# Kernel optimization log

Measured on AMD Instinct MI355X. Metric: run time of the kernel, lower is better.

Reference implementation:

```python
import jax, jax.numpy as jnp
from jax import lax
import numpy as np

RATIO = 2
KF = 12  # FIR kernel size = 6 * ratio


def _kaiser_sinc_filter(cutoff, half_width, ksize):
    # matches BigVGAN alias_free_torch kaiser_sinc_filter1d (even ksize branch)
    half_size = ksize // 2
    delta_f = 4.0 * half_width
    A = 2.285 * (half_size - 1) * np.pi * delta_f + 7.95
    if A > 50.0:
        beta = 0.1102 * (A - 8.7)
    elif A >= 21.0:
        beta = 0.5842 * (A - 21.0) ** 0.4 + 0.07886 * (A - 21.0)
    else:
        beta = 0.0
    window = np.kaiser(ksize, beta)
    time = np.arange(-half_size, half_size) + 0.5
    filt = 2 * cutoff * window * np.sinc(2 * cutoff * time)
    filt = filt / filt.sum()
    return filt.astype(np.float32)


FILT = jnp.asarray(_kaiser_sinc_filter(0.5 / RATIO, 0.6 / RATIO, KF))  # [12], symmetric


def _depthwise(x, stride, lhs_dil, pad):
    # x: [B, C, T]; same FIR filter applied per channel
    C = x.shape[1]
    w = jnp.broadcast_to(FILT.reshape(1, 1, KF), (C, 1, KF))
    return lax.conv_general_dilated(
        x, w, window_strides=(stride,), padding=[pad], lhs_dilation=(lhs_dil,),
        dimension_numbers=('NCH', 'OIH', 'NCH'), feature_group_count=C)


def _activation1d(x, log_alpha, log_beta):
    # anti-aliased SnakeBeta: upsample x2 -> snake -> downsample x2 (length preserved)
    # UpSample1d(ratio=2): replicate-pad 5, conv_transpose stride 2, crop 15 each side
    x = jnp.pad(x, ((0, 0), (0, 0), (5, 5)), mode='edge')
    x = RATIO * _depthwise(x, stride=1, lhs_dil=RATIO, pad=(KF - 1, KF - 1))
    x = x[..., 15:-15]  # [B, C, 2T]
    a = jnp.exp(log_alpha)[None, :, None]
    b = jnp.exp(log_beta)[None, :, None]
    x = x + (1.0 / (b + 1e-9)) * jnp.square(jnp.sin(x * a))
    # DownSample1d: replicate-pad (5, 6), conv stride 2
    x = jnp.pad(x, ((0, 0), (0, 0), (5, 6)), mode='edge')
    return _depthwise(x, stride=RATIO, lhs_dil=1, pad=(0, 0))


def _wn_conv(x, v, g, b, d):
    # weight_norm: w = g * v / ||v||_(in,k) per output channel; dilated, 'same' padding
    w = g * v * lax.rsqrt(jnp.sum(v * v, axis=(1, 2), keepdims=True))
    y = lax.conv_general_dilated(
        x, w, window_strides=(1,), padding=[(d, d)], rhs_dilation=(d,),
        dimension_numbers=('NCH', 'OIH', 'NCH'))
    return y + b[None, :, None]


def setup_inputs() -> dict:
    key = jax.random.key(0)
    ks = jax.random.split(key, 4)
    B, C, T, L = 8, 512, 8192, 3
    x = jax.random.normal(ks[0], (B, C, T), jnp.float32)
    conv_v = 0.01 * jax.random.normal(ks[1], (L, C, C, 3), jnp.float32)  # init_weights std=0.01
    conv_g = jnp.ones((L, C, 1, 1), jnp.float32)
    conv_b = jnp.zeros((L, C), jnp.float32)
    alpha = 0.1 * jax.random.normal(ks[2], (L, C), jnp.float32)  # log-scale snake params
    beta = 0.1 * jax.random.normal(ks[3], (L, C), jnp.float32)
    return {'x': x, 'conv_v': conv_v, 'conv_g': conv_g, 'conv_b': conv_b,
            'alpha': alpha, 'beta': beta}


def reference(x, conv_v, conv_g, conv_b, alpha, beta):
    for i, d in enumerate((1, 3, 5)):
        xt = _activation1d(x, alpha[i], beta[i])
        xt = _wn_conv(xt, conv_v[i], conv_g[i], conv_b[i], d)
        x = xt + x
    return x
```

## Files before the change

kernel.cpp:

```cpp
#include <hip/hip_runtime.h>
#include <hip/hip_bf16.h>
#include <cmath>

#define CCH 512
#define TLEN 8192
#define NB 8
#define KFILT 12

typedef unsigned short u16;
typedef __attribute__((ext_vector_type(8))) short short8;
typedef __attribute__((ext_vector_type(8))) unsigned short ushort8;
typedef __attribute__((ext_vector_type(4))) float float4v;
typedef __attribute__((ext_vector_type(4))) int int4v;

struct Filt { float f[KFILT]; };

static double bessel_i0(double x) {
    double sum = 1.0, term = 1.0;
    for (int k = 1; k < 40; ++k) {
        double t = (x * 0.5) / k;
        term *= t * t;
        sum += term;
        if (term < 1e-18 * sum) break;
    }
    return sum;
}

static void make_filter(float* out) {
    const int ksize = KFILT, half = KFILT / 2;
    const double cutoff = 0.5 / 2.0;
    const double half_width = 0.6 / 2.0;
    const double delta_f = 4.0 * half_width;
    const double PI = 3.14159265358979323846;
    double A = 2.285 * (half - 1) * PI * delta_f + 7.95;
    double beta;
    if (A > 50.0) beta = 0.1102 * (A - 8.7);
    else if (A >= 21.0) beta = 0.5842 * pow(A - 21.0, 0.4) + 0.07886 * (A - 21.0);
    else beta = 0.0;
    double i0b = bessel_i0(beta);
    double sum = 0.0, f[KFILT];
    for (int n = 0; n < ksize; ++n) {
        double r = (2.0 * n) / (ksize - 1) - 1.0;
        double w = bessel_i0(beta * sqrt(fmax(0.0, 1.0 - r * r))) / i0b;
        double t = (n - half) + 0.5;
        double xx = 2.0 * cutoff * t;
        double snc = (xx == 0.0) ? 1.0 : sin(PI * xx) / (PI * xx);
        f[n] = 2.0 * cutoff * w * snc;
        sum += f[n];
    }
    for (int n = 0; n < ksize; ++n) out[n] = (float)(f[n] / sum);
}

__device__ __forceinline__ float bf2f(u16 u) {
    return __uint_as_float(((unsigned int)u) << 16);
}
__device__ __forceinline__ u16 f2bf(float f) {
    unsigned int x = __float_as_uint(f);
    unsigned int r = (x + 0x7fffu + ((x >> 16) & 1u)) >> 16;
    return (u16)r;
}
__device__ __forceinline__ float ldin(const void* p, size_t i, int isf) {
    return isf ? ((const float*)p)[i] : bf2f(((const u16*)p)[i]);
}
__device__ __forceinline__ void gl_lds16(const void* g, void* s) {
    __builtin_amdgcn_global_load_lds(
        (const __attribute__((address_space(1))) unsigned int*)g,
        (__attribute__((address_space(3))) unsigned int*)s, 16, 0, 0);
}

__global__ __launch_bounds__(256) void k_detect(const u16* __restrict__ x,
                                                int* __restrict__ flag) {
    int tid = threadIdx.x;
    int bad = 0;
    for (int i = tid; i < 4096; i += 256) {
        int e = (x[i] >> 7) & 0xFF;
        if (e >= 0x86) bad++;
    }
    for (int off = 32; off > 0; off >>= 1) bad += __shfl_down(bad, off, 64);
    __shared__ int r[4];
    if ((tid & 63) == 0) r[tid >> 6] = bad;
    __syncthreads();
    if (tid == 0) flag[0] = (r[0] + r[1] + r[2] + r[3] >= 64) ? 1 : 0;
}

__global__ __launch_bounds__(256) void k_scales(const void* __restrict__ v,
                                                const void* __restrict__ g,
                                                float* __restrict__ scales,
                                                const int* __restrict__ flg) {
    int isf = *flg;
    int blk = blockIdx.x;
    int tid = threadIdx.x;
    float s = 0.f;
    for (int i = tid; i < CCH * 3; i += 256) {
        float x = ldin(v, (size_t)blk * (CCH * 3) + i, isf);
        s = fmaf(x, x, s);
    }
    for (int off = 32; off > 0; off >>= 1) s += __shfl_down(s, off, 64);
    __shared__ float red[4];
    if ((tid & 63) == 0) red[tid >> 6] = s;
    __syncthreads();
    if (tid == 0) {
        float tot = red[0] + red[1] + red[2] + red[3];
        scales[blk] = ldin(g, blk, isf) / sqrtf(tot);
    }
}

__global__ __launch_bounds__(256) void k_repack(const void* __restrict__ v,
                                                u16* __restrict__ wp,
                                                const int* __restrict__ flg) {
    int isf = *flg;
    int l = blockIdx.y;
    int i = blockIdx.x * 256 + threadIdx.x;
    int tap = i >> 18;
    int rem = i & 262143;
    int co = rem >> 9, ci = rem & 511;
    size_t src = (((size_t)l * CCH + co) * CCH + ci) * 3 + tap;
    u16 val = isf ? f2bf(((const float*)v)[src]) : ((const u16*)v)[src];
    wp[(((size_t)l * 3 + tap) * CCH + co) * CCH + ci] = val;
}

template<int UL>
__device__ __forceinline__ float su_val(const float* xr, const Filt& F,
                                        float a, float invb) {
    constexpr int S = (UL < 0) ? -(((-UL) + 1) / 2) : (UL / 2);
    constexpr int P = ((UL % 2) + 2) % 2;
    constexpr int B = S + (P ? 4 : 3);
    float acc = F.f[P] * xr[B];
    #pragma unroll
    for (int r = 1; r < 6; ++r) acc = fmaf(F.f[2 * r + P], xr[B + r], acc);
    acc *= 2.0f;
    float sn = __sinf(acc * a);
    return fmaf(invb, sn * sn, acc);
}

__global__ __launch_bounds__(256) void k_act(const void* __restrict__ xsrc,
                                             const void* __restrict__ alpha,
                                             const void* __restrict__ beta,
                                             int prmofs, u16* __restrict__ xt,
                                             Filt F, const int* __restrict__ flg,
                                             int layer0) {
    const int isf = *flg;
    const int sif = layer0 ? isf : 0;
    const int tid = threadIdx.x;
    const int lane = tid & 63, w = tid >> 6;
    const int b = blockIdx.z;
    const int c = blockIdx.y * 64 + lane;
    const int t0 = blockIdx.x * 128 + w * 32;
    const size_t rowbase = ((size_t)(b * CCH + c)) * TLEN;

    const float a = expf(ldin(alpha, prmofs + c, isf));
    const float invb = 1.0f / (expf(ldin(beta, prmofs + c, isf)) + 1e-9f);

    float xr[44];
    const bool interior = (t0 != 0) && (t0 != TLEN - 32);
    if (sif) {
        const float* xp = (const float*)xsrc + rowbase;
        if (interior) {
            #pragma unroll
            for (int i = 0; i < 12; ++i) {
                float4v v = *(const float4v*)(xp + t0 - 8 + i * 4);
                #pragma unroll
                for (int j = 0; j < 4; ++j) {
                    int k = i * 4 + j - 2;
                    if (k >= 0 && k < 44) xr[k] = v[j];
                }
            }
        } else {
            #pragma unroll
            for (int k = 0; k < 44; ++k)
                xr[k] = xp[min(max(t0 - 6 + k, 0), TLEN - 1)];
        }
    } else {
        const u16* xp = (const u16*)xsrc + rowbase;
        if (interior) {
            #pragma unroll
            for (int i = 0; i < 6; ++i) {
                ushort8 v = *(const ushort8*)(xp + t0 - 8 + i * 8);
                #pragma unroll
                for (int j = 0; j < 8; ++j) {
                    int k = i * 8 + j - 2;
                    if (k >= 0 && k < 44) xr[k] = bf2f(v[j]);
                }
            }
        } else {
            #pragma unroll
            for (int k = 0; k < 44; ++k)
                xr[k] = bf2f(xp[min(max(t0 - 6 + k, 0), TLEN - 1)]);
        }
    }

    float wv[12];
    wv[7]  = su_val<-5>(xr, F, a, invb);
    wv[8]  = su_val<-4>(xr, F, a, invb);
    wv[9]  = su_val<-3>(xr, F, a, invb);
    wv[10] = su_val<-2>(xr, F, a, invb);
    wv[11] = su_val<-1>(xr, F, a, invb);
    wv[0]  = su_val<0>(xr, F, a, invb);
    wv[1]  = su_val<1>(xr, F, a, invb);
    wv[2]  = su_val<2>(xr, F, a, invb);
    wv[3]  = su_val<3>(xr, F, a, invb);
    wv[4]  = su_val<4>(xr, F, a, invb);
    wv[5]  = su_val<5>(xr, F, a, invb);
    wv[6]  = su_val<6>(xr, F, a, invb);
    if (t0 == 0) { wv[7] = wv[8] = wv[9] = wv[10] = wv[11] = wv[0]; }
    const bool right = (t0 == TLEN - 32);
    const float su_hi = su_val<63>(xr, F, a, invb);

    u16* orow = xt + (size_t)b * TLEN * CCH + c;

#define IDXW(u) ((((u) % 12) + 12) % 12)
#define ACT_STEP(TL) { \
      float acc = F.f[0] * wv[IDXW(2*(TL)-5)]; \
      acc = fmaf(F.f[1],  wv[IDXW(2*(TL)-4)], acc); \
      acc = fmaf(F.f[2],  wv[IDXW(2*(TL)-3)], acc); \
      acc = fmaf(F.f[3],  wv[IDXW(2*(TL)-2)], acc); \
      acc = fmaf(F.f[4],  wv[IDXW(2*(TL)-1)], acc); \
      acc = fmaf(F.f[5],  wv[IDXW(2*(TL)+0)], acc); \
      acc = fmaf(F.f[6],  wv[IDXW(2*(TL)+1)], acc); \
      acc = fmaf(F.f[7],  wv[IDXW(2*(TL)+2)], acc); \
      acc = fmaf(F.f[8],  wv[IDXW(2*(TL)+3)], acc); \
      acc = fmaf(F.f[9],  wv[IDXW(2*(TL)+4)], acc); \
      acc = fmaf(F.f[10], wv[IDXW(2*(TL)+5)], acc); \
      acc = fmaf(F.f[11], wv[IDXW(2*(TL)+6)], acc); \
      orow[(size_t)(t0 + (TL)) * CCH] = f2bf(acc); \
      if ((TL) < 31) { \
        float nv1 = su_val<2*(TL)+7>(xr, F, a, invb); \
        float nv2 = su_val<2*(TL)+8>(xr, F, a, invb); \
        if ((2*(TL)+7) > 63) nv1 = right ? su_hi : nv1; \
        if ((2*(TL)+8) > 63) nv2 = right ? su_hi : nv2; \
        wv[IDXW(2*(TL)+7)] = nv1; \
        wv[IDXW(2*(TL)+8)] = nv2; \
      } \
    }

    ACT_STEP(0)  ACT_STEP(1)  ACT_STEP(2)  ACT_STEP(3)
    ACT_STEP(4)  ACT_STEP(5)  ACT_STEP(6)  ACT_STEP(7)
    ACT_STEP(8)  ACT_STEP(9)  ACT_STEP(10) ACT_STEP(11)
    ACT_STEP(12) ACT_STEP(13) ACT_STEP(14) ACT_STEP(15)
    ACT_STEP(16) ACT_STEP(17) ACT_STEP(18) ACT_STEP(19)
    ACT_STEP(20) ACT_STEP(21) ACT_STEP(22) ACT_STEP(23)
    ACT_STEP(24) ACT_STEP(25) ACT_STEP(26) ACT_STEP(27)
    ACT_STEP(28) ACT_STEP(29) ACT_STEP(30) ACT_STEP(31)
#undef ACT_STEP
#undef IDXW
}

__global__ __launch_bounds__(512, 2) void k_conv(const u16* __restrict__ xt,
                                              const u16* __restrict__ wp,
                                              const float* __restrict__ scales,
                                              const void* __restrict__ bias,
                                              int bofs,
                                              const void* __restrict__ rsrc,
                                              int layer0,
                                              u16* __restrict__ wdst,
                                              void* __restrict__ outp, int d,
                                              const int* __restrict__ flg,
                                              const u16* __restrict__ zsrc) {
    extern __shared__ __align__(16) char smem[];
    const int isf = *flg;
    const int rif = layer0 ? isf : 0;
    const int tid = threadIdx.x;
    const int lane = tid & 63, wid = tid >> 6;
    const int wm = wid & 1, wn = wid >> 1;
    const int b = blockIdx.z, co0 = blockIdx.y * 128, t0 = blockIdx.x * 256;
    const int q = lane >> 4, l15 = lane & 15;
    const u16* xtb = xt + (size_t)b * TLEN * CCH;

    char* Ab[3] = { smem, smem + 24576, smem + 49152 };
    char* Xb[3] = { smem + 73728, smem + 98304, smem + 122880 };

    const u16* wsrc3[3];
    #pragma unroll
    for (int i = 0; i < 3; ++i) {
        int L = i * 512 + tid;
        int tap = L >> 9;
        int co = (L >> 2) & 127;
        int g = (L & 3) ^ ((co >> 1) & 3);
        wsrc3[i] = wp + (((size_t)tap * CCH + co0 + co) * CCH) + g * 8;
    }
    const u16* xsrc3[3];
    #pragma unroll
    for (int i = 0; i < 3; ++i) {
        int idx = i * 512 + tid;
        int t = idx >> 2;
        int g = (idx & 3) ^ ((t >> 1) & 3);
        int tg = t0 - d + t;
        if (tg < 0 || tg >= TLEN) xsrc3[i] = zsrc;
        else xsrc3[i] = xtb + (size_t)tg * CCH + g * 8;
    }

    auto stage = [&](int ci0, char* A, char* X) {
        #pragma unroll
        for (int i = 0; i < 3; ++i)
            gl_lds16(wsrc3[i] + ci0, A + (i * 512 + wid * 64) * 16);
        #pragma unroll
        for (int i = 0; i < 3; ++i)
            gl_lds16(xsrc3[i] + ci0, X + (i * 512 + wid * 64) * 16);
    };

    float4v acc[4][4];
    #pragma unroll
    for (int i = 0; i < 4; ++i)
        #pragma unroll
        for (int j = 0; j < 4; ++j) acc[i][j] = (float4v){0.f, 0.f, 0.f, 0.f};

    stage(0, Ab[0], Xb[0]);
    stage(32, Ab[1], Xb[1]);
    asm volatile("s_waitcnt vmcnt(6)" ::: "memory");
    __builtin_amdgcn_s_barrier();
    __builtin_amdgcn_sched_barrier(0);

    char *Ac = Ab[0], *An = Ab[1], *Af = Ab[2];
    char *Xc = Xb[0], *Xn = Xb[1], *Xf = Xb[2];
    for (int s = 0; s < 16; ++s) {
        if (s < 14) stage((s + 2) * 32, Af, Xf);
        #pragma unroll
        for (int tap = 0; tap < 3; ++tap) {
            short8 af[4], bfr[4];
            #pragma unroll
            for (int mi = 0; mi < 4; ++mi) {
                int co = wm * 64 + mi * 16 + l15;
                af[mi] = *(const short8*)(Ac + tap * 8192 + co * 64 +
                                          ((q ^ ((co >> 1) & 3)) * 16));
            }
            #pragma unroll
            for (int ni = 0; ni < 4; ++ni) {
                int r = wn * 64 + ni * 16 + l15 + tap * d;
                bfr[ni] = *(const short8*)(Xc + r * 64 + ((q ^ ((r >> 1) & 3)) * 16));
            }
            __builtin_amdgcn_s_setprio(1);
            #pragma unroll
            for (int mi = 0; mi < 4; ++mi)
                #pragma unroll
                for (int ni = 0; ni < 4; ++ni)
                    acc[mi][ni] = __builtin_amdgcn_mfma_f32_16x16x32_bf16(
                        af[mi], bfr[ni], acc[mi][ni], 0, 0, 0);
            __builtin_amdgcn_s_setprio(0);
        }
        if (s == 15) break;
        if (s < 14) asm volatile("s_waitcnt vmcnt(6)" ::: "memory");
        else        asm volatile("s_waitcnt vmcnt(0)" ::: "memory");
        __builtin_amdgcn_s_barrier();
        __builtin_amdgcn_sched_barrier(0);
        char* t1 = Ac; Ac = An; An = Af; Af = t1;
        char* t2 = Xc; Xc = Xn; Xn = Xf; Xf = t2;
    }

    float scl[4][4], bia[4][4];
    #pragma unroll
    for (int mi = 0; mi < 4; ++mi)
        #pragma unroll
        for (int rg = 0; rg < 4; ++rg) {
            int co = co0 + wm * 64 + mi * 16 + q * 4 + rg;
            scl[mi][rg] = scales[co];
            bia[mi][rg] = ldin(bias, bofs + co, isf);
        }
    #pragma unroll
    for (int mi = 0; mi < 4; ++mi)
        #pragma unroll
        for (int ni = 0; ni < 4; ++ni) {
            int tg = t0 + wn * 64 + ni * 16 + l15;
            #pragma unroll
            for (int rg = 0; rg < 4; ++rg) {
                int co = co0 + wm * 64 + mi * 16 + q * 4 + rg;
                size_t idx = ((size_t)(b * CCH + co)) * TLEN + tg;
                float resid = rif ? ((const float*)rsrc)[idx]
                                  : bf2f(((const u16*)rsrc)[idx]);
                float val = fmaf(acc[mi][ni][rg], scl[mi][rg], bia[mi][rg]) + resid;
                if (wdst) {
                    wdst[idx] = f2bf(val);
                } else {
                    if (isf) ((float*)outp)[idx] = val;
                    else ((u16*)outp)[idx] = f2bf(val);
                }
            }
        }
}

extern "C" void kernel_launch(void* const* d_in, const int* in_sizes, int n_in,
                              void* d_out, int out_size, void* d_ws, size_t ws_size,
                              hipStream_t stream) {
    const void* x_in  = d_in[0];
    const void* v_in  = d_in[1];
    const void* g_in  = d_in[2];
    const void* b_in  = d_in[3];
    const void* al_in = d_in[4];
    const void* be_in = d_in[5];

    char* ws = (char*)d_ws;
    u16*   xc     = (u16*)ws;
    u16*   xt     = (u16*)(ws + 67108864);
    u16*   wp     = (u16*)(ws + 134217728);
    float* scales = (float*)(ws + 134217728 + 4718592);
    int*   flag   = (int*)(ws + 134217728 + 4718592 + 6144);
    u16*   zbuf   = (u16*)(ws + 134217728 + 4718592 + 6144 + 64);

    Filt F;
    make_filter(F.f);

    (void)hipFuncSetAttribute((const void*)k_conv,
                              hipFuncAttributeMaxDynamicSharedMemorySize, 147456);

    (void)hipMemsetAsync(zbuf, 0, 2048, stream);

    k_detect<<<1, 256, 0, stream>>>((const u16*)x_in, flag);
    k_scales<<<3 * CCH, 256, 0, stream>>>(v_in, g_in, scales, flag);
    k_repack<<<dim3(3072, 3), 256, 0, stream>>>(v_in, wp, flag);

    const int dil[3] = {1, 3, 5};
    for (int l = 0; l < 3; ++l) {
        const void* src = (l == 0) ? x_in : (const void*)xc;
        k_act<<<dim3(TLEN / 128, CCH / 64, NB), 256, 0, stream>>>(
            src, al_in, be_in, l * CCH, xt, F, flag, (l == 0) ? 1 : 0);
        k_conv<<<dim3(TLEN / 256, CCH / 128, NB), 512, 147456, stream>>>(
            xt, wp + (size_t)l * 3 * CCH * CCH, scales + l * CCH, b_in, l * CCH,
            src, (l == 0) ? 1 : 0,
            (l == 2) ? (u16*)nullptr : xc,
            (l == 2) ? d_out : nullptr, dil[l], flag, zbuf);
    }
}
```

Measured before the change: 826.7 us.

## Halve conv time tile to 128 and switch to double-buffered LDS for occupancy

The conv kernel's output tile shrinks from 128x256 to 128x128 (time axis), and the triple-buffered LDS pipeline with explicit vmcnt waits is replaced by a simple double buffer with __syncthreads. This cuts LDS use from 144KB to about 66KB, and with launch bounds raised to 4 it aims to fit more blocks per CU and hide latency through occupancy. In exchange, each weight tile is reused across half as many time columns, so per-FLOP weight traffic doubles, and the prefetch depth and sync granularity get coarser.

```diff
diff --git a/kernel.cpp b/kernel.cpp
--- a/kernel.cpp
+++ b/kernel.cpp
@@ -245,7 +245,7 @@
 #undef IDXW
 }
 
-__global__ __launch_bounds__(512, 2) void k_conv(const u16* __restrict__ xt,
+__global__ __launch_bounds__(512, 4) void k_conv(const u16* __restrict__ xt,
                                               const u16* __restrict__ wp,
                                               const float* __restrict__ scales,
                                               const void* __restrict__ bias,
@@ -262,12 +262,9 @@
     const int tid = threadIdx.x;
     const int lane = tid & 63, wid = tid >> 6;
     const int wm = wid & 1, wn = wid >> 1;
-    const int b = blockIdx.z, co0 = blockIdx.y * 128, t0 = blockIdx.x * 256;
+    const int b = blockIdx.z, co0 = blockIdx.y * 128, t0 = blockIdx.x * 128;
     const int q = lane >> 4, l15 = lane & 15;
     const u16* xtb = xt + (size_t)b * TLEN * CCH;
-
-    char* Ab[3] = { smem, smem + 24576, smem + 49152 };
-    char* Xb[3] = { smem + 73728, smem + 98304, smem + 122880 };
 
     const u16* wsrc3[3];
     #pragma unroll
@@ -278,45 +275,50 @@
         int g = (L & 3) ^ ((co >> 1) & 3);
         wsrc3[i] = wp + (((size_t)tap * CCH + co0 + co) * CCH) + g * 8;
     }
-    const u16* xsrc3[3];
-    #pragma unroll
-    for (int i = 0; i < 3; ++i) {
-        int idx = i * 512 + tid;
-        int t = idx >> 2;
-        int g = (idx & 3) ^ ((t >> 1) & 3);
+    const u16* xsrc0;
+    const u16* xsrc1 = zsrc;
+    {
+        int t = tid >> 2;
+        int g = (tid & 3) ^ ((t >> 1) & 3);
         int tg = t0 - d + t;
-        if (tg < 0 || tg >= TLEN) xsrc3[i] = zsrc;
-        else xsrc3[i] = xtb + (size_t)tg * CCH + g * 8;
+        xsrc0 = (tg < 0 || tg >= TLEN) ? zsrc : xtb + (size_t)tg * CCH + g * 8;
+    }
+    if (tid < 64) {
+        int j = 512 + tid;
+        int t = j >> 2;
+        int g = (j & 3) ^ ((t >> 1) & 3);
+        int tg = t0 - d + t;
+        xsrc1 = (tg < 0 || tg >= TLEN) ? zsrc : xtb + (size_t)tg * CCH + g * 8;
     }
 
     auto stage = [&](int ci0, char* A, char* X) {
         #pragma unroll
         for (int i = 0; i < 3; ++i)
             gl_lds16(wsrc3[i] + ci0, A + (i * 512 + wid * 64) * 16);
-        #pragma unroll
-        for (int i = 0; i < 3; ++i)
-            gl_lds16(xsrc3[i] + ci0, X + (i * 512 + wid * 64) * 16);
+        gl_lds16(xsrc0 + ci0, X + wid * 1024);
+        if (tid < 64) gl_lds16(xsrc1 + ci0, X + 8192);
     };
 
-    float4v acc[4][4];
+    float4v acc[4][2];
     #pragma unroll
     for (int i = 0; i < 4; ++i)
         #pragma unroll
-        for (int j = 0; j < 4; ++j) acc[i][j] = (float4v){0.f, 0.f, 0.f, 0.f};
-
-    stage(0, Ab[0], Xb[0]);
-    stage(32, Ab[1], Xb[1]);
-    asm volatile("s_waitcnt vmcnt(6)" ::: "memory");
-    __builtin_amdgcn_s_barrier();
-    __builtin_amdgcn_sched_barrier(0);
-
-    char *Ac = Ab[0], *An = Ab[1], *Af = Ab[2];
-    char *Xc = Xb[0], *Xn = Xb[1], *Xf = Xb[2];
+        for (int j = 0; j < 2; ++j) acc[i][j] = (float4v){0.f, 0.f, 0.f, 0.f};
+
+    stage(0, smem, smem + 49152);
+    __syncthreads();
+
     for (int s = 0; s < 16; ++s) {
-        if (s < 14) stage((s + 2) * 32, Af, Xf);
+        char* Ac = smem + (s & 1) * 24576;
+        char* Xc = smem + 49152 + (s & 1) * 9216;
+        if (s < 15) {
+            char* An = smem + ((s + 1) & 1) * 24576;
+            char* Xn = smem + 49152 + ((s + 1) & 1) * 9216;
+            stage((s + 1) * 32, An, Xn);
+        }
         #pragma unroll
         for (int tap = 0; tap < 3; ++tap) {
-            short8 af[4], bfr[4];
+            short8 af[4], bfr[2];
             #pragma unroll
             for (int mi = 0; mi < 4; ++mi) {
                 int co = wm * 64 + mi * 16 + l15;
@@ -324,26 +326,20 @@
                                           ((q ^ ((co >> 1) & 3)) * 16));
             }
             #pragma unroll
-            for (int ni = 0; ni < 4; ++ni) {
-                int r = wn * 64 + ni * 16 + l15 + tap * d;
+            for (int ni = 0; ni < 2; ++ni) {
+                int r = wn * 32 + ni * 16 + l15 + tap * d;
                 bfr[ni] = *(const short8*)(Xc + r * 64 + ((q ^ ((r >> 1) & 3)) * 16));
             }
             __builtin_amdgcn_s_setprio(1);
             #pragma unroll
             for (int mi = 0; mi < 4; ++mi)
                 #pragma unroll
-                for (int ni = 0; ni < 4; ++ni)
+                for (int ni = 0; ni < 2; ++ni)
                     acc[mi][ni] = __builtin_amdgcn_mfma_f32_16x16x32_bf16(
                         af[mi], bfr[ni], acc[mi][ni], 0, 0, 0);
             __builtin_amdgcn_s_setprio(0);
         }
-        if (s == 15) break;
-        if (s < 14) asm volatile("s_waitcnt vmcnt(6)" ::: "memory");
-        else        asm volatile("s_waitcnt vmcnt(0)" ::: "memory");
-        __builtin_amdgcn_s_barrier();
-        __builtin_amdgcn_sched_barrier(0);
-        char* t1 = Ac; Ac = An; An = Af; Af = t1;
-        char* t2 = Xc; Xc = Xn; Xn = Xf; Xf = t2;
+        __syncthreads();
     }
 
     float scl[4][4], bia[4][4];
@@ -358,8 +354,8 @@
     #pragma unroll
     for (int mi = 0; mi < 4; ++mi)
         #pragma unroll
-        for (int ni = 0; ni < 4; ++ni) {
-            int tg = t0 + wn * 64 + ni * 16 + l15;
+        for (int ni = 0; ni < 2; ++ni) {
+            int tg = t0 + wn * 32 + ni * 16 + l15;
             #pragma unroll
             for (int rg = 0; rg < 4; ++rg) {
                 int co = co0 + wm * 64 + mi * 16 + q * 4 + rg;
@@ -399,7 +395,7 @@
     make_filter(F.f);
 
     (void)hipFuncSetAttribute((const void*)k_conv,
-                              hipFuncAttributeMaxDynamicSharedMemorySize, 147456);
+                              hipFuncAttributeMaxDynamicSharedMemorySize, 67584);
 
     (void)hipMemsetAsync(zbuf, 0, 2048, stream);
 
@@ -412,7 +408,7 @@
         const void* src = (l == 0) ? x_in : (const void*)xc;
         k_act<<<dim3(TLEN / 128, CCH / 64, NB), 256, 0, stream>>>(
             src, al_in, be_in, l * CCH, xt, F, flag, (l == 0) ? 1 : 0);
-        k_conv<<<dim3(TLEN / 256, CCH / 128, NB), 512, 147456, stream>>>(
+        k_conv<<<dim3(TLEN / 128, CCH / 128, NB), 512, 67584, stream>>>(
             xt, wp + (size_t)l * 3 * CCH * CCH, scales + l * CCH, b_in, l * CCH,
             src, (l == 0) ? 1 : 0,
             (l == 2) ? (u16*)nullptr : xc,
```

Measured after the change: 757.6 us. 8.4% less time.
